# Kernel tuning notes

Measured on AMD Instinct MI355X. Metric: run time of the kernel, lower is better.

Reference implementation:

```python
import jax, jax.numpy as jnp
import numpy as np

N_NODES = 100000
N_EDGES = 1600000
N_GRAPHS = 512
IN_DIM, HID_DIM, OUT_DIM = 128, 256, 128
EPS = 0.0  # PyG GINConv default eps (train_eps=False)


def setup_inputs() -> dict:
    key = jax.random.key(0)
    ks = jax.random.split(key, 9)
    x = jax.random.normal(ks[0], (N_NODES, IN_DIM), dtype=jnp.float32)
    edge_index = jax.random.randint(ks[1], (2, N_EDGES), 0, N_NODES, dtype=jnp.int64)
    batch_ids = jnp.sort(jax.random.randint(ks[2], (N_NODES,), 0, N_GRAPHS, dtype=jnp.int64))
    s1 = 1.0 / np.sqrt(IN_DIM)
    s2 = 1.0 / np.sqrt(HID_DIM)
    W1 = jax.random.normal(ks[3], (IN_DIM, HID_DIM), dtype=jnp.float32) * s1
    b1 = jax.random.normal(ks[4], (HID_DIM,), dtype=jnp.float32) * s1
    W2 = jax.random.normal(ks[5], (HID_DIM, HID_DIM), dtype=jnp.float32) * s2
    b2 = jax.random.normal(ks[6], (HID_DIM,), dtype=jnp.float32) * s2
    Wo = jax.random.normal(ks[7], (HID_DIM, OUT_DIM), dtype=jnp.float32) * s2
    bo = jax.random.normal(ks[8], (OUT_DIM,), dtype=jnp.float32) * s2
    return {"x": x, "edge_index": edge_index, "batch_ids": batch_ids,
            "W1": W1, "b1": b1, "W2": W2, "b2": b2, "Wo": Wo, "bo": bo}


def reference(x, edge_index, batch_ids, W1, b1, W2, b2, Wo, bo):
    src, dst = edge_index[0], edge_index[1]
    # GIN aggregation: sum of neighbor features scattered to destination nodes
    agg = jax.ops.segment_sum(x[src], dst, num_segments=N_NODES)  # [N, in]
    h = (1.0 + EPS) * x + agg
    # GIN MLP: Linear -> ReLU -> Linear -> ReLU
    h = jax.nn.relu(h @ W1 + b1)
    h = jax.nn.relu(h @ W2 + b2)
    out = h @ Wo + bo  # output_layer
    # global_add_pool over graphs
    pooled = jax.ops.segment_sum(out, batch_ids, num_segments=N_GRAPHS)  # [G, out]
    return pooled
```

## Files before the change

### kernel.cpp

```cpp
#include <hip/hip_runtime.h>

#define N_NODES  100000
#define M_PAD    100096
#define N_EDGES  1600000
#define N_GRAPHS 512
#define IN_DIM   128
#define HID_DIM  256
#define OUT_DIM  128

#define NB       782
#define BCAP     3072
#define CHUNK    2048
#define BKB      ((N_EDGES + CHUNK - 1) / CHUNK)

typedef __bf16 bf16x8 __attribute__((ext_vector_type(8)));
typedef __bf16 bf16x4 __attribute__((ext_vector_type(4)));
typedef __bf16 bf16x2 __attribute__((ext_vector_type(2)));
typedef float  f32x4  __attribute__((ext_vector_type(4)));

#define WP_L2_BASE 32768
#define WP_L3_BASE 98304
#define WP_TOTAL   131072

#define R_X    (N_NODES * IN_DIM / 4)
#define R_APAD ((M_PAD - N_NODES) * IN_DIM / 4)
#define R_WP   WP_TOTAL
#define R_OUT  (N_GRAPHS * OUT_DIM / 4)
#define R_CUR  NB
#define R_TOTAL (R_X + R_APAD + R_WP + R_OUT + R_CUR)

__global__ __launch_bounds__(256) void init_kernel(const float* __restrict__ x,
                                                   const float* __restrict__ W1,
                                                   const float* __restrict__ W2,
                                                   const float* __restrict__ Wo,
                                                   __bf16* __restrict__ xb,
                                                   __bf16* __restrict__ Apad,
                                                   __bf16* __restrict__ Wp,
                                                   float* __restrict__ outbuf,
                                                   int* __restrict__ gcursor) {
    long long i = (long long)blockIdx.x * blockDim.x + threadIdx.x;
    if (i < R_X) {
        float4 v = ((const float4*)x)[i];
        bf16x4 h;
        h.x = (__bf16)v.x; h.y = (__bf16)v.y; h.z = (__bf16)v.z; h.w = (__bf16)v.w;
        ((bf16x4*)xb)[i] = h;
        return;
    }
    i -= R_X;
    if (i < R_APAD) {
        bf16x4 z; z.x = (__bf16)0.f; z.y = (__bf16)0.f; z.z = (__bf16)0.f; z.w = (__bf16)0.f;
        ((bf16x4*)Apad)[i] = z;
        return;
    }
    i -= R_APAD;
    if (i < R_WP) {
        int idx = (int)i;
        const float* src;
        int K, Nn, base;
        if (idx < WP_L2_BASE)      { src = W1; K = 128; Nn = 256; base = 0; }
        else if (idx < WP_L3_BASE) { src = W2; K = 256; Nn = 256; base = WP_L2_BASE; }
        else                       { src = Wo; K = 256; Nn = 128; base = WP_L3_BASE; }
        int r0 = idx - base;
        int slabElems = 32 * K;
        int j = r0 / slabElems;
        int r = r0 % slabElems;
        int KS = K / 32;
        int p = r >> 9;
        int lane = (r >> 3) & 63;
        int e = r & 7;
        int s = p % KS, t = p / KS;
        int quad = lane >> 4, l16 = lane & 15;
        int n = j * 32 + t * 16 + l16;
        int k = s * 32 + quad * 8 + e;
        Wp[idx] = (__bf16)src[(size_t)k * Nn + n];
        return;
    }
    i -= R_WP;
    if (i < R_OUT) {
        ((float4*)outbuf)[i] = make_float4(0.f, 0.f, 0.f, 0.f);
        return;
    }
    i -= R_OUT;
    if (i < R_CUR) gcursor[i] = 0;
}

__global__ __launch_bounds__(256) void bucket_v2_kernel(const int* __restrict__ ei,
                                                        int* __restrict__ gcursor,
                                                        unsigned* __restrict__ pairBuf) {
    __shared__ int lcnt[NB];
    __shared__ int lbase[NB];
    const int tid = threadIdx.x;
    const int e0 = blockIdx.x * CHUNK;

    for (int b = tid; b < NB; b += 256) lcnt[b] = 0;
    __syncthreads();

    for (int i = tid; i < CHUNK; i += 256) {
        int e = e0 + i;
        if (e < N_EDGES) atomicAdd(&lcnt[ei[N_EDGES + e] >> 7], 1);
    }
    __syncthreads();

    for (int b = tid; b < NB; b += 256) {
        int c = lcnt[b];
        lbase[b] = c ? atomicAdd(&gcursor[b], c) : 0;
        lcnt[b] = 0;
    }
    __syncthreads();

    for (int i = tid; i < CHUNK; i += 256) {
        int e = e0 + i;
        if (e < N_EDGES) {
            int s = ei[e];
            int d = ei[N_EDGES + e];
            int b = d >> 7;
            int pos = lbase[b] + atomicAdd(&lcnt[b], 1);
            if (pos < BCAP)
                pairBuf[(size_t)b * BCAP + pos] = (unsigned)s | ((unsigned)(d & 127) << 17);
        }
    }
}

__global__ __launch_bounds__(256) void passB_kernel(const unsigned* __restrict__ pairBuf,
                                                    const int* __restrict__ gcursor,
                                                    int* __restrict__ nbr,
                                                    int* __restrict__ offsets,
                                                    int* __restrict__ deg) {
    __shared__ int lcnt[128];
    __shared__ int loffs[128];
    __shared__ int lcur[128];
    const int b = blockIdx.x;
    const int tid = threadIdx.x;
    const int node0 = b << 7;
    const int cnt = min(gcursor[b], BCAP);
    const int base = b * BCAP;
    const unsigned* pb = pairBuf + (size_t)b * BCAP;

    if (tid < 128) { lcnt[tid] = 0; lcur[tid] = 0; }
    __syncthreads();

    for (int i = tid; i < cnt; i += 256)
        atomicAdd(&lcnt[pb[i] >> 17], 1);
    __syncthreads();

    if (tid < 128) loffs[tid] = lcnt[tid];
    __syncthreads();
    for (int st = 1; st < 128; st <<= 1) {
        int add = (tid < 128 && tid >= st) ? loffs[tid - st] : 0;
        __syncthreads();
        if (tid < 128) loffs[tid] += add;
        __syncthreads();
    }
    int excl = 0;
    if (tid < 128) {
        excl = loffs[tid] - lcnt[tid];
        int node = node0 + tid;
        if (node < N_NODES) {
            deg[node] = lcnt[tid];
            offsets[node] = base + excl;
        }
    }
    __syncthreads();
    if (tid < 128) loffs[tid] = excl;
    __syncthreads();

    for (int i = tid; i < cnt; i += 256) {
        unsigned u = pb[i];
        int dl = u >> 17;
        int slot = atomicAdd(&lcur[dl], 1);
        nbr[base + loffs[dl] + slot] = (int)(u & 0x1FFFF);
    }
}

__global__ __launch_bounds__(256) void aggregate_kernel(const __bf16* __restrict__ xb,
                                                        const int* __restrict__ offsets,
                                                        const int* __restrict__ deg,
                                                        const int* __restrict__ nbr,
                                                        __bf16* __restrict__ A) {
    int v = blockIdx.x * 4 + (threadIdx.x >> 6);
    v = __builtin_amdgcn_readfirstlane(v);
    int lane = threadIdx.x & 63;
    if (v >= N_NODES) return;
    int off = offsets[v];
    int len = deg[v];
    const int c0 = lane * 2;
    bf16x2 self = *(const bf16x2*)(xb + (size_t)v * IN_DIM + c0);
    float ax = (float)self.x, ay = (float)self.y;

    int addr = off + lane;
    if (addr > NB * BCAP - 1) addr = NB * BCAP - 1;
    int myidx = nbr[addr];

    int lim = len < 64 ? len : 64;
    int j = 0;
    for (; j + 8 <= lim; j += 8) {
        int s0 = __shfl(myidx, j + 0, 64);
        int s1 = __shfl(myidx, j + 1, 64);
        int s2 = __shfl(myidx, j + 2, 64);
        int s3 = __shfl(myidx, j + 3, 64);
        int s4 = __shfl(myidx, j + 4, 64);
        int s5 = __shfl(myidx, j + 5, 64);
        int s6 = __shfl(myidx, j + 6, 64);
        int s7 = __shfl(myidx, j + 7, 64);
        bf16x2 v0 = *(const bf16x2*)(xb + (size_t)s0 * IN_DIM + c0);
        bf16x2 v1 = *(const bf16x2*)(xb + (size_t)s1 * IN_DIM + c0);
        bf16x2 v2 = *(const bf16x2*)(xb + (size_t)s2 * IN_DIM + c0);
        bf16x2 v3 = *(const bf16x2*)(xb + (size_t)s3 * IN_DIM + c0);
        bf16x2 v4 = *(const bf16x2*)(xb + (size_t)s4 * IN_DIM + c0);
        bf16x2 v5 = *(const bf16x2*)(xb + (size_t)s5 * IN_DIM + c0);
        bf16x2 v6 = *(const bf16x2*)(xb + (size_t)s6 * IN_DIM + c0);
        bf16x2 v7 = *(const bf16x2*)(xb + (size_t)s7 * IN_DIM + c0);
        ax += (float)v0.x + (float)v1.x + (float)v2.x + (float)v3.x
            + (float)v4.x + (float)v5.x + (float)v6.x + (float)v7.x;
        ay += (float)v0.y + (float)v1.y + (float)v2.y + (float)v3.y
            + (float)v4.y + (float)v5.y + (float)v6.y + (float)v7.y;
    }
    for (; j < lim; ++j) {
        int s = __shfl(myidx, j, 64);
        bf16x2 vv = *(const bf16x2*)(xb + (size_t)s * IN_DIM + c0);
        ax += (float)vv.x;
        ay += (float)vv.y;
    }
    for (; j < len; ++j) {
        int s = nbr[off + j];
        bf16x2 vv = *(const bf16x2*)(xb + (size_t)s * IN_DIM + c0);
        ax += (float)vv.x;
        ay += (float)vv.y;
    }
    bf16x2 h;
    h.x = (__bf16)ax;
    h.y = (__bf16)ay;
    *(bf16x2*)(A + (size_t)v * IN_DIM + c0) = h;
}

__device__ __forceinline__ void load_group_p(const __bf16* __restrict__ p, int lane,
                                             bf16x8* __restrict__ dst) {
    #pragma unroll
    for (int e = 0; e < 8; ++e)
        dst[e] = *(const bf16x8*)(p + (e * 64 + lane) * 8);
}

__device__ __forceinline__ void store_H(__bf16* __restrict__ H, int j, int quad, int l16,
                                        const f32x4 (&acc)[2][2], float bt0, float bt1) {
    const int c7 = l16 & 7;
    const int ch = l16 >> 3;
    #pragma unroll
    for (int i = 0; i < 2; ++i)
        #pragma unroll
        for (int t = 0; t < 2; ++t) {
            const float bb = t ? bt1 : bt0;
            #pragma unroll
            for (int rr = 0; rr < 4; ++rr) {
                int row = i * 16 + quad * 4 + rr;
                int cidx = (j * 4 + t * 2 + ch + row) & 31;
                float v = fmaxf(acc[i][t][rr] + bb, 0.f);
                H[row * 256 + cidx * 8 + c7] = (__bf16)v;
            }
        }
}

__global__ __launch_bounds__(64) void mlp_fused(const __bf16* __restrict__ A,
                                                const __bf16* __restrict__ Wp,
                                                const float* __restrict__ b1,
                                                const float* __restrict__ b2,
                                                const float* __restrict__ bo,
                                                float* __restrict__ out,
                                                const int* __restrict__ batch) {
    __shared__ __bf16 H[32 * 256];

    const int lane = threadIdx.x;
    const int quad = lane >> 4, l16 = lane & 15;
    const size_t mblk = (size_t)blockIdx.x * 32;
    const int r0g = (int)mblk;
    int gfirst = (r0g < N_NODES) ? batch[r0g] : -2;
    int glast  = (r0g + 31 < N_NODES) ? batch[r0g + 31] : -1;

    bf16x8 a[2][8];
    bf16x8 buf0[8];
    bf16x8 buf1[8];

    const __bf16* wp = Wp;
    load_group_p(wp, lane, buf0);

    #pragma unroll
    for (int i = 0; i < 2; ++i)
        #pragma unroll
        for (int s = 0; s < 4; ++s)
            a[i][s] = *(const bf16x8*)(A + (mblk + i * 16 + l16) * IN_DIM + s * 32 + quad * 8);

    #pragma unroll 1
    for (int j = 0; j < 8; j += 2) {
        {
            load_group_p(wp + 4096, lane, buf1);
            float bt0 = b1[j * 32 + l16];
            float bt1 = b1[j * 32 + 16 + l16];
            f32x4 acc[2][2] = {};
            #pragma unroll
            for (int p = 0; p < 8; ++p) {
                const int t = p >> 2, s = p & 3;
                acc[0][t] = __builtin_amdgcn_mfma_f32_16x16x32_bf16(a[0][s], buf0[p], acc[0][t], 0, 0, 0);
                acc[1][t] = __builtin_amdgcn_mfma_f32_16x16x32_bf16(a[1][s], buf0[p], acc[1][t], 0, 0, 0);
            }
            store_H(H, j, quad, l16, acc, bt0, bt1);
        }
        {
            load_group_p(wp + 8192, lane, buf0);
            float bt0 = b1[(j + 1) * 32 + l16];
            float bt1 = b1[(j + 1) * 32 + 16 + l16];
            f32x4 acc[2][2] = {};
            #pragma unroll
            for (int p = 0; p < 8; ++p) {
                const int t = p >> 2, s = p & 3;
                acc[0][t] = __builtin_amdgcn_mfma_f32_16x16x32_bf16(a[0][s], buf1[p], acc[0][t], 0, 0, 0);
                acc[1][t] = __builtin_amdgcn_mfma_f32_16x16x32_bf16(a[1][s], buf1[p], acc[1][t], 0, 0, 0);
            }
            store_H(H, j + 1, quad, l16, acc, bt0, bt1);
        }
        wp += 8192;
    }
    __syncthreads();

    #pragma unroll
    for (int i = 0; i < 2; ++i)
        #pragma unroll
        for (int s = 0; s < 8; ++s) {
            int row = i * 16 + l16;
            a[i][s] = *(const bf16x8*)(H + row * 256 + (((s * 4 + quad) + row) & 31) * 8);
        }
    __syncthreads();

    #pragma unroll 1
    for (int j = 0; j < 8; ++j) {
        load_group_p(wp + 4096, lane, buf1);
        float bt0 = b2[j * 32 + l16];
        float bt1 = b2[j * 32 + 16 + l16];
        f32x4 acc[2][2] = {};
        #pragma unroll
        for (int p = 0; p < 8; ++p) {
            acc[0][0] = __builtin_amdgcn_mfma_f32_16x16x32_bf16(a[0][p], buf0[p], acc[0][0], 0, 0, 0);
            acc[1][0] = __builtin_amdgcn_mfma_f32_16x16x32_bf16(a[1][p], buf0[p], acc[1][0], 0, 0, 0);
        }
        load_group_p(wp + 8192, lane, buf0);
        #pragma unroll
        for (int p = 0; p < 8; ++p) {
            acc[0][1] = __builtin_amdgcn_mfma_f32_16x16x32_bf16(a[0][p], buf1[p], acc[0][1], 0, 0, 0);
            acc[1][1] = __builtin_amdgcn_mfma_f32_16x16x32_bf16(a[1][p], buf1[p], acc[1][1], 0, 0, 0);
        }
        store_H(H, j, quad, l16, acc, bt0, bt1);
        wp += 8192;
    }
    __syncthreads();

    #pragma unroll
    for (int i = 0; i < 2; ++i)
        #pragma unroll
        for (int s = 0; s < 8; ++s) {
            int row = i * 16 + l16;
            a[i][s] = *(const bf16x8*)(H + row * 256 + (((s * 4 + quad) + row) & 31) * 8);
        }

    #pragma unroll 1
    for (int j = 0; j < 4; ++j) {
        load_group_p(wp + 4096, lane, buf1);
        float bt0 = bo[j * 32 + l16];
        float bt1 = bo[j * 32 + 16 + l16];
        f32x4 acc[2][2] = {};
        #pragma unroll
        for (int p = 0; p < 8; ++p) {
            acc[0][0] = __builtin_amdgcn_mfma_f32_16x16x32_bf16(a[0][p], buf0[p], acc[0][0], 0, 0, 0);
            acc[1][0] = __builtin_amdgcn_mfma_f32_16x16x32_bf16(a[1][p], buf0[p], acc[1][0], 0, 0, 0);
        }
        load_group_p(wp + 8192, lane, buf0);
        #pragma unroll
        for (int p = 0; p < 8; ++p) {
            acc[0][1] = __builtin_amdgcn_mfma_f32_16x16x32_bf16(a[0][p], buf1[p], acc[0][1], 0, 0, 0);
            acc[1][1] = __builtin_amdgcn_mfma_f32_16x16x32_bf16(a[1][p], buf1[p], acc[1][1], 0, 0, 0);
        }

        if (gfirst == glast) {
            #pragma unroll
            for (int t = 0; t < 2; ++t) {
                float sum = 0.f;
                #pragma unroll
                for (int i = 0; i < 2; ++i)
                    #pragma unroll
                    for (int rr = 0; rr < 4; ++rr) sum += acc[i][t][rr];
                sum += __shfl_xor(sum, 16, 64);
                sum += __shfl_xor(sum, 32, 64);
                if (quad == 0) {
                    int c = j * 32 + t * 16 + l16;
                    float bb = t ? bt1 : bt0;
                    atomicAdd(out + (size_t)gfirst * OUT_DIM + c, sum + 32.f * bb);
                }
            }
        } else {
            #pragma unroll
            for (int i = 0; i < 2; ++i)
                #pragma unroll
                for (int rr = 0; rr < 4; ++rr) {
                    int m = r0g + i * 16 + quad * 4 + rr;
                    if (m < N_NODES) {
                        int g = batch[m];
                        #pragma unroll
                        for (int t = 0; t < 2; ++t) {
                            int c = j * 32 + t * 16 + l16;
                            float bb = t ? bt1 : bt0;
                            atomicAdd(out + (size_t)g * OUT_DIM + c, acc[i][t][rr] + bb);
                        }
                    }
                }
        }
        wp += 8192;
    }
}

extern "C" void kernel_launch(void* const* d_in, const int* in_sizes, int n_in,
                              void* d_out, int out_size, void* d_ws, size_t ws_size,
                              hipStream_t stream) {
    const float* x  = (const float*)d_in[0];
    const int*   ei = (const int*)d_in[1];
    const int*   bi = (const int*)d_in[2];
    const float* W1 = (const float*)d_in[3];
    const float* b1 = (const float*)d_in[4];
    const float* W2 = (const float*)d_in[5];
    const float* b2 = (const float*)d_in[6];
    const float* Wo = (const float*)d_in[7];
    const float* bo = (const float*)d_in[8];
    float* out = (float*)d_out;

    __bf16* A  = (__bf16*)d_ws;
    __bf16* xb = A + (size_t)M_PAD * IN_DIM;
    __bf16* Wp = xb + (size_t)N_NODES * IN_DIM;
    unsigned* pairBuf = (unsigned*)(Wp + WP_TOTAL);
    int* nbr      = (int*)(pairBuf + (size_t)NB * BCAP);
    int* offsets  = nbr + (size_t)NB * BCAP;
    int* deg      = offsets + N_NODES;
    int* gcursor  = deg + N_NODES;

    init_kernel<<<(R_TOTAL + 255) / 256, 256, 0, stream>>>(
        x, W1, W2, Wo, xb, A + (size_t)N_NODES * IN_DIM, Wp, out, gcursor);

    bucket_v2_kernel<<<BKB, 256, 0, stream>>>(ei, gcursor, pairBuf);
    passB_kernel<<<NB, 256, 0, stream>>>(pairBuf, gcursor, nbr, offsets, deg);

    aggregate_kernel<<<(N_NODES + 3) / 4, 256, 0, stream>>>(xb, offsets, deg, nbr, A);

    mlp_fused<<<M_PAD / 32, 64, 0, stream>>>(A, Wp, b1, b2, bo, out, bi);
}
```

Baseline: 290.0 us.

## Stage MLP weights through shared memory and widen row tiles per wave

The fused MLP kernel now uses two waves per block, each handling 64 rows instead of 32. Weight fragments are cooperatively loaded into a double-buffered LDS ring, with __syncthreads between stages, instead of every wave loading them straight from global memory. This is meant to halve weight traffic per row and to reuse each fragment across more MFMAs. In exchange it roughly doubles register use for A fragments and accumulators, and adds a block barrier on every weight stage.

New measurement: 336.5 us. +16.0%, slower.

```diff
diff --git a/kernel.cpp b/kernel.cpp
--- a/kernel.cpp
+++ b/kernel.cpp
@@ -233,19 +233,59 @@
     *(bf16x2*)(A + (size_t)v * IN_DIM + c0) = h;
 }
 
-__device__ __forceinline__ void load_group_p(const __bf16* __restrict__ p, int lane,
-                                             bf16x8* __restrict__ dst) {
+#define MLP_ROWS_W  64
+#define MLP_WAVES   2
+#define MLP_ROWS_B  (MLP_ROWS_W * MLP_WAVES)
+
+__device__ __forceinline__ void stage_issue(const __bf16* __restrict__ g, int wid, int lane,
+                                            bf16x8* __restrict__ r) {
+    const __bf16* p = g + wid * 2048 + lane * 8;
+    #pragma unroll
+    for (int c = 0; c < 4; ++c)
+        r[c] = *(const bf16x8*)(p + c * 512);
+}
+
+__device__ __forceinline__ void stage_write(__bf16* __restrict__ lb, int wid, int lane,
+                                            const bf16x8* __restrict__ r) {
+    __bf16* p = lb + wid * 2048 + lane * 8;
+    #pragma unroll
+    for (int c = 0; c < 4; ++c)
+        *(bf16x8*)(p + c * 512) = r[c];
+}
+
+__device__ __forceinline__ void read_frags(const __bf16* __restrict__ lb, int lane,
+                                           bf16x8* __restrict__ f) {
     #pragma unroll
     for (int e = 0; e < 8; ++e)
-        dst[e] = *(const bf16x8*)(p + (e * 64 + lane) * 8);
+        f[e] = *(const bf16x8*)(lb + (e * 64 + lane) * 8);
+}
+
+__device__ __forceinline__ void mfma_L1(const bf16x8 (&a)[4][8], const bf16x8* __restrict__ f,
+                                        f32x4 (&acc)[4][2]) {
+    #pragma unroll
+    for (int p = 0; p < 8; ++p) {
+        const int t = p >> 2, s = p & 3;
+        #pragma unroll
+        for (int i = 0; i < 4; ++i)
+            acc[i][t] = __builtin_amdgcn_mfma_f32_16x16x32_bf16(a[i][s], f[p], acc[i][t], 0, 0, 0);
+    }
+}
+
+__device__ __forceinline__ void mfma_K256(const bf16x8 (&a)[4][8], const bf16x8* __restrict__ f,
+                                          f32x4 (&acc)[4][2], int t) {
+    #pragma unroll
+    for (int p = 0; p < 8; ++p)
+        #pragma unroll
+        for (int i = 0; i < 4; ++i)
+            acc[i][t] = __builtin_amdgcn_mfma_f32_16x16x32_bf16(a[i][p], f[p], acc[i][t], 0, 0, 0);
 }
 
 __device__ __forceinline__ void store_H(__bf16* __restrict__ H, int j, int quad, int l16,
-                                        const f32x4 (&acc)[2][2], float bt0, float bt1) {
+                                        const f32x4 (&acc)[4][2], float bt0, float bt1) {
     const int c7 = l16 & 7;
     const int ch = l16 >> 3;
     #pragma unroll
-    for (int i = 0; i < 2; ++i)
+    for (int i = 0; i < 4; ++i)
         #pragma unroll
         for (int t = 0; t < 2; ++t) {
             const float bb = t ? bt1 : bt0;
@@ -259,130 +299,116 @@
         }
 }
 
-__global__ __launch_bounds__(64) void mlp_fused(const __bf16* __restrict__ A,
-                                                const __bf16* __restrict__ Wp,
-                                                const float* __restrict__ b1,
-                                                const float* __restrict__ b2,
-                                                const float* __restrict__ bo,
-                                                float* __restrict__ out,
-                                                const int* __restrict__ batch) {
-    __shared__ __bf16 H[32 * 256];
-
-    const int lane = threadIdx.x;
+__global__ __launch_bounds__(128, 1) void mlp_fused(const __bf16* __restrict__ A,
+                                                    const __bf16* __restrict__ Wp,
+                                                    const float* __restrict__ b1,
+                                                    const float* __restrict__ b2,
+                                                    const float* __restrict__ bo,
+                                                    float* __restrict__ out,
+                                                    const int* __restrict__ batch) {
+    __shared__ __align__(16) __bf16 H[MLP_ROWS_B * 256];
+    __shared__ __align__(16) __bf16 WB[2][4096];
+
+    const int tid  = threadIdx.x;
+    const int wid  = tid >> 6;
+    const int lane = tid & 63;
     const int quad = lane >> 4, l16 = lane & 15;
-    const size_t mblk = (size_t)blockIdx.x * 32;
+    __bf16* Hw = H + wid * MLP_ROWS_W * 256;
+
+    const size_t mblk = (size_t)blockIdx.x * MLP_ROWS_B + wid * MLP_ROWS_W;
     const int r0g = (int)mblk;
     int gfirst = (r0g < N_NODES) ? batch[r0g] : -2;
-    int glast  = (r0g + 31 < N_NODES) ? batch[r0g + 31] : -1;
-
-    bf16x8 a[2][8];
-    bf16x8 buf0[8];
-    bf16x8 buf1[8];
-
-    const __bf16* wp = Wp;
-    load_group_p(wp, lane, buf0);
-
-    #pragma unroll
-    for (int i = 0; i < 2; ++i)
+    int glast  = (r0g + 63 < N_NODES) ? batch[r0g + 63] : -1;
+
+    bf16x8 a[4][8];
+    bf16x8 f[8];
+    bf16x8 st[4];
+
+    stage_issue(Wp, wid, lane, st);
+    #pragma unroll
+    for (int i = 0; i < 4; ++i)
         #pragma unroll
         for (int s = 0; s < 4; ++s)
             a[i][s] = *(const bf16x8*)(A + (mblk + i * 16 + l16) * IN_DIM + s * 32 + quad * 8);
+    stage_write(WB[0], wid, lane, st);
+    __syncthreads();
+
+    const __bf16* wp = Wp;
 
     #pragma unroll 1
-    for (int j = 0; j < 8; j += 2) {
-        {
-            load_group_p(wp + 4096, lane, buf1);
-            float bt0 = b1[j * 32 + l16];
-            float bt1 = b1[j * 32 + 16 + l16];
-            f32x4 acc[2][2] = {};
-            #pragma unroll
-            for (int p = 0; p < 8; ++p) {
-                const int t = p >> 2, s = p & 3;
-                acc[0][t] = __builtin_amdgcn_mfma_f32_16x16x32_bf16(a[0][s], buf0[p], acc[0][t], 0, 0, 0);
-                acc[1][t] = __builtin_amdgcn_mfma_f32_16x16x32_bf16(a[1][s], buf0[p], acc[1][t], 0, 0, 0);
-            }
-            store_H(H, j, quad, l16, acc, bt0, bt1);
-        }
-        {
-            load_group_p(wp + 8192, lane, buf0);
-            float bt0 = b1[(j + 1) * 32 + l16];
-            float bt1 = b1[(j + 1) * 32 + 16 + l16];
-            f32x4 acc[2][2] = {};
-            #pragma unroll
-            for (int p = 0; p < 8; ++p) {
-                const int t = p >> 2, s = p & 3;
-                acc[0][t] = __builtin_amdgcn_mfma_f32_16x16x32_bf16(a[0][s], buf1[p], acc[0][t], 0, 0, 0);
-                acc[1][t] = __builtin_amdgcn_mfma_f32_16x16x32_bf16(a[1][s], buf1[p], acc[1][t], 0, 0, 0);
-            }
-            store_H(H, j + 1, quad, l16, acc, bt0, bt1);
-        }
-        wp += 8192;
-    }
-    __syncthreads();
-
-    #pragma unroll
-    for (int i = 0; i < 2; ++i)
+    for (int j = 0; j < 8; ++j) {
+        stage_issue(wp + 4096, wid, lane, st);
+        read_frags(WB[j & 1], lane, f);
+        float bt0 = b1[j * 32 + l16];
+        float bt1 = b1[j * 32 + 16 + l16];
+        f32x4 acc[4][2] = {};
+        mfma_L1(a, f, acc);
+        store_H(Hw, j, quad, l16, acc, bt0, bt1);
+        stage_write(WB[(j + 1) & 1], wid, lane, st);
+        __syncthreads();
+        wp += 4096;
+    }
+
+    #pragma unroll
+    for (int i = 0; i < 4; ++i)
         #pragma unroll
         for (int s = 0; s < 8; ++s) {
             int row = i * 16 + l16;
-            a[i][s] = *(const bf16x8*)(H + row * 256 + (((s * 4 + quad) + row) & 31) * 8);
-        }
-    __syncthreads();
+            a[i][s] = *(const bf16x8*)(Hw + row * 256 + (((s * 4 + quad) + row) & 31) * 8);
+        }
 
     #pragma unroll 1
     for (int j = 0; j < 8; ++j) {
-        load_group_p(wp + 4096, lane, buf1);
+        f32x4 acc[4][2] = {};
+        stage_issue(wp + 4096, wid, lane, st);
+        read_frags(WB[0], lane, f);
+        mfma_K256(a, f, acc, 0);
+        stage_write(WB[1], wid, lane, st);
+        __syncthreads();
+        wp += 4096;
+        stage_issue(wp + 4096, wid, lane, st);
+        read_frags(WB[1], lane, f);
+        mfma_K256(a, f, acc, 1);
+        stage_write(WB[0], wid, lane, st);
+        __syncthreads();
+        wp += 4096;
         float bt0 = b2[j * 32 + l16];
         float bt1 = b2[j * 32 + 16 + l16];
-        f32x4 acc[2][2] = {};
-        #pragma unroll
-        for (int p = 0; p < 8; ++p) {
-            acc[0][0] = __builtin_amdgcn_mfma_f32_16x16x32_bf16(a[0][p], buf0[p], acc[0][0], 0, 0, 0);
-            acc[1][0] = __builtin_amdgcn_mfma_f32_16x16x32_bf16(a[1][p], buf0[p], acc[1][0], 0, 0, 0);
-        }
-        load_group_p(wp + 8192, lane, buf0);
-        #pragma unroll
-        for (int p = 0; p < 8; ++p) {
-            acc[0][1] = __builtin_amdgcn_mfma_f32_16x16x32_bf16(a[0][p], buf1[p], acc[0][1], 0, 0, 0);
-            acc[1][1] = __builtin_amdgcn_mfma_f32_16x16x32_bf16(a[1][p], buf1[p], acc[1][1], 0, 0, 0);
-        }
-        store_H(H, j, quad, l16, acc, bt0, bt1);
-        wp += 8192;
-    }
-    __syncthreads();
-
-    #pragma unroll
-    for (int i = 0; i < 2; ++i)
+        store_H(Hw, j, quad, l16, acc, bt0, bt1);
+    }
+
+    #pragma unroll
+    for (int i = 0; i < 4; ++i)
         #pragma unroll
         for (int s = 0; s < 8; ++s) {
             int row = i * 16 + l16;
-            a[i][s] = *(const bf16x8*)(H + row * 256 + (((s * 4 + quad) + row) & 31) * 8);
+            a[i][s] = *(const bf16x8*)(Hw + row * 256 + (((s * 4 + quad) + row) & 31) * 8);
         }
 
     #pragma unroll 1
     for (int j = 0; j < 4; ++j) {
-        load_group_p(wp + 4096, lane, buf1);
+        f32x4 acc[4][2] = {};
+        stage_issue(wp + 4096, wid, lane, st);
+        read_frags(WB[0], lane, f);
+        mfma_K256(a, f, acc, 0);
+        stage_write(WB[1], wid, lane, st);
+        __syncthreads();
+        wp += 4096;
+        stage_issue(wp + 4096, wid, lane, st);
+        read_frags(WB[1], lane, f);
+        mfma_K256(a, f, acc, 1);
+        stage_write(WB[0], wid, lane, st);
+        __syncthreads();
+        wp += 4096;
         float bt0 = bo[j * 32 + l16];
         float bt1 = bo[j * 32 + 16 + l16];
-        f32x4 acc[2][2] = {};
-        #pragma unroll
-        for (int p = 0; p < 8; ++p) {
-            acc[0][0] = __builtin_amdgcn_mfma_f32_16x16x32_bf16(a[0][p], buf0[p], acc[0][0], 0, 0, 0);
-            acc[1][0] = __builtin_amdgcn_mfma_f32_16x16x32_bf16(a[1][p], buf0[p], acc[1][0], 0, 0, 0);
-        }
-        load_group_p(wp + 8192, lane, buf0);
-        #pragma unroll
-        for (int p = 0; p < 8; ++p) {
-            acc[0][1] = __builtin_amdgcn_mfma_f32_16x16x32_bf16(a[0][p], buf1[p], acc[0][1], 0, 0, 0);
-            acc[1][1] = __builtin_amdgcn_mfma_f32_16x16x32_bf16(a[1][p], buf1[p], acc[1][1], 0, 0, 0);
-        }
 
         if (gfirst == glast) {
             #pragma unroll
             for (int t = 0; t < 2; ++t) {
                 float sum = 0.f;
                 #pragma unroll
-                for (int i = 0; i < 2; ++i)
+                for (int i = 0; i < 4; ++i)
                     #pragma unroll
                     for (int rr = 0; rr < 4; ++rr) sum += acc[i][t][rr];
                 sum += __shfl_xor(sum, 16, 64);
@@ -390,12 +416,12 @@
                 if (quad == 0) {
                     int c = j * 32 + t * 16 + l16;
                     float bb = t ? bt1 : bt0;
-                    atomicAdd(out + (size_t)gfirst * OUT_DIM + c, sum + 32.f * bb);
+                    atomicAdd(out + (size_t)gfirst * OUT_DIM + c, sum + 64.f * bb);
                 }
             }
         } else {
             #pragma unroll
-            for (int i = 0; i < 2; ++i)
+            for (int i = 0; i < 4; ++i)
                 #pragma unroll
                 for (int rr = 0; rr < 4; ++rr) {
                     int m = r0g + i * 16 + quad * 4 + rr;
@@ -410,7 +436,6 @@
                     }
                 }
         }
-        wp += 8192;
     }
 }
 
@@ -445,5 +470,5 @@
 
     aggregate_kernel<<<(N_NODES + 3) / 4, 256, 0, stream>>>(xb, offsets, deg, nbr, A);
 
-    mlp_fused<<<M_PAD / 32, 64, 0, stream>>>(A, Wp, b1, b2, bo, out, bi);
-}
+    mlp_fused<<<M_PAD / MLP_ROWS_B, MLP_WAVES * 64, 0, stream>>>(A, Wp, b1, b2, bo, out, bi);
+}
```

## Pack four waves per MLP block and deepen weight prefetch to two groups

Applied to the files above, without the earlier changes.

The fused MLP kernel now runs four independent waves per 256-thread block, each with its own 32-row slice and private LDS tile, instead of one 64-thread wave per block. Weight fragments are triple or quad buffered in registers so each step loads the groups two steps ahead, hiding global/L2 latency behind the MFMAs. The goal is fewer, larger blocks and more latency hiding. The cost is higher register pressure (launch bounds 256,2) and 64KB of LDS per block, which may limit occupancy. M_PAD is evenly divisible by 128, so the grid still covers every row.

New measurement: 298.3 us. 2.9% more time.

```diff
diff --git a/kernel.cpp b/kernel.cpp
--- a/kernel.cpp
+++ b/kernel.cpp
@@ -233,8 +233,12 @@
     *(bf16x2*)(A + (size_t)v * IN_DIM + c0) = h;
 }
 
-__device__ __forceinline__ void load_group_p(const __bf16* __restrict__ p, int lane,
-                                             bf16x8* __restrict__ dst) {
+#define MLP_WAVES   4
+#define MLP_ROWS_W  32
+#define MLP_ROWS_B  (MLP_WAVES * MLP_ROWS_W)
+
+__device__ __forceinline__ void load_group4(const __bf16* __restrict__ p, int lane,
+                                            bf16x8* __restrict__ dst) {
     #pragma unroll
     for (int e = 0; e < 8; ++e)
         dst[e] = *(const bf16x8*)(p + (e * 64 + lane) * 8);
@@ -259,65 +263,60 @@
         }
 }
 
-__global__ __launch_bounds__(64) void mlp_fused(const __bf16* __restrict__ A,
-                                                const __bf16* __restrict__ Wp,
-                                                const float* __restrict__ b1,
-                                                const float* __restrict__ b2,
-                                                const float* __restrict__ bo,
-                                                float* __restrict__ out,
-                                                const int* __restrict__ batch) {
-    __shared__ __bf16 H[32 * 256];
-
-    const int lane = threadIdx.x;
+__global__ __launch_bounds__(256, 2) void mlp_fused(const __bf16* __restrict__ A,
+                                                    const __bf16* __restrict__ Wp,
+                                                    const float* __restrict__ b1,
+                                                    const float* __restrict__ b2,
+                                                    const float* __restrict__ bo,
+                                                    float* __restrict__ out,
+                                                    const int* __restrict__ batch) {
+    __shared__ __align__(16) __bf16 H[MLP_WAVES][32 * 256];
+
+    const int tid  = threadIdx.x;
+    const int wid  = tid >> 6;
+    const int lane = tid & 63;
     const int quad = lane >> 4, l16 = lane & 15;
-    const size_t mblk = (size_t)blockIdx.x * 32;
+    __bf16* Hw = H[wid];
+
+    const size_t mblk = (size_t)blockIdx.x * MLP_ROWS_B + wid * MLP_ROWS_W;
     const int r0g = (int)mblk;
     int gfirst = (r0g < N_NODES) ? batch[r0g] : -2;
     int glast  = (r0g + 31 < N_NODES) ? batch[r0g + 31] : -1;
 
     bf16x8 a[2][8];
-    bf16x8 buf0[8];
-    bf16x8 buf1[8];
-
-    const __bf16* wp = Wp;
-    load_group_p(wp, lane, buf0);
-
+    bf16x8 w0[8], w1[8], w2[8], w3[8];
+
+    load_group4(Wp, lane, w0);
+    load_group4(Wp + 4096, lane, w1);
     #pragma unroll
     for (int i = 0; i < 2; ++i)
         #pragma unroll
         for (int s = 0; s < 4; ++s)
             a[i][s] = *(const bf16x8*)(A + (mblk + i * 16 + l16) * IN_DIM + s * 32 + quad * 8);
 
+#define L1_BODY(J, CW, PW)                                                              \
+    {                                                                                   \
+        load_group4(Wp + (size_t)((J) + 2) * 4096, lane, PW);                           \
+        float bt0 = b1[(J) * 32 + l16];                                                 \
+        float bt1 = b1[(J) * 32 + 16 + l16];                                            \
+        f32x4 acc[2][2] = {};                                                           \
+        _Pragma("unroll")                                                               \
+        for (int p = 0; p < 8; ++p) {                                                   \
+            const int t = p >> 2, s = p & 3;                                            \
+            acc[0][t] = __builtin_amdgcn_mfma_f32_16x16x32_bf16(a[0][s], CW[p], acc[0][t], 0, 0, 0); \
+            acc[1][t] = __builtin_amdgcn_mfma_f32_16x16x32_bf16(a[1][s], CW[p], acc[1][t], 0, 0, 0); \
+        }                                                                               \
+        store_H(Hw, (J), quad, l16, acc, bt0, bt1);                                     \
+    }
+
     #pragma unroll 1
-    for (int j = 0; j < 8; j += 2) {
-        {
-            load_group_p(wp + 4096, lane, buf1);
-            float bt0 = b1[j * 32 + l16];
-            float bt1 = b1[j * 32 + 16 + l16];
-            f32x4 acc[2][2] = {};
-            #pragma unroll
-            for (int p = 0; p < 8; ++p) {
-                const int t = p >> 2, s = p & 3;
-                acc[0][t] = __builtin_amdgcn_mfma_f32_16x16x32_bf16(a[0][s], buf0[p], acc[0][t], 0, 0, 0);
-                acc[1][t] = __builtin_amdgcn_mfma_f32_16x16x32_bf16(a[1][s], buf0[p], acc[1][t], 0, 0, 0);
-            }
-            store_H(H, j, quad, l16, acc, bt0, bt1);
-        }
-        {
-            load_group_p(wp + 8192, lane, buf0);
-            float bt0 = b1[(j + 1) * 32 + l16];
-            float bt1 = b1[(j + 1) * 32 + 16 + l16];
-            f32x4 acc[2][2] = {};
-            #pragma unroll
-            for (int p = 0; p < 8; ++p) {
-                const int t = p >> 2, s = p & 3;
-                acc[0][t] = __builtin_amdgcn_mfma_f32_16x16x32_bf16(a[0][s], buf1[p], acc[0][t], 0, 0, 0);
-                acc[1][t] = __builtin_amdgcn_mfma_f32_16x16x32_bf16(a[1][s], buf1[p], acc[1][t], 0, 0, 0);
-            }
-            store_H(H, j + 1, quad, l16, acc, bt0, bt1);
-        }
-        wp += 8192;
-    }
+    for (int j = 0; j < 8; j += 4) {
+        L1_BODY(j + 0, w0, w2)
+        L1_BODY(j + 1, w1, w3)
+        L1_BODY(j + 2, w2, w0)
+        L1_BODY(j + 3, w3, w1)
+    }
+#undef L1_BODY
     __syncthreads();
 
     #pragma unroll
@@ -325,29 +324,34 @@
         #pragma unroll
         for (int s = 0; s < 8; ++s) {
             int row = i * 16 + l16;
-            a[i][s] = *(const bf16x8*)(H + row * 256 + (((s * 4 + quad) + row) & 31) * 8);
+            a[i][s] = *(const bf16x8*)(Hw + row * 256 + (((s * 4 + quad) + row) & 31) * 8);
         }
-    __syncthreads();
+
+#define K256_BODY(GB, J, CE, CO, PE, PO, BIAS, TAIL)                                    \
+    {                                                                                   \
+        const __bf16* pf = Wp + (size_t)((GB) + 2 * (J) + 2) * 4096;                    \
+        load_group4(pf, lane, PE);                                                      \
+        load_group4(pf + 4096, lane, PO);                                               \
+        float bt0 = BIAS[(J) * 32 + l16];                                               \
+        float bt1 = BIAS[(J) * 32 + 16 + l16];                                          \
+        f32x4 acc[2][2] = {};                                                           \
+        _Pragma("unroll")                                                               \
+        for (int p = 0; p < 8; ++p) {                                                   \
+            acc[0][0] = __builtin_amdgcn_mfma_f32_16x16x32_bf16(a[0][p], CE[p], acc[0][0], 0, 0, 0); \
+            acc[1][0] = __builtin_amdgcn_mfma_f32_16x16x32_bf16(a[1][p], CE[p], acc[1][0], 0, 0, 0); \
+        }                                                                               \
+        _Pragma("unroll")                                                               \
+        for (int p = 0; p < 8; ++p) {                                                   \
+            acc[0][1] = __builtin_amdgcn_mfma_f32_16x16x32_bf16(a[0][p], CO[p], acc[0][1], 0, 0, 0); \
+            acc[1][1] = __builtin_amdgcn_mfma_f32_16x16x32_bf16(a[1][p], CO[p], acc[1][1], 0, 0, 0); \
+        }                                                                               \
+        TAIL                                                                            \
+    }
 
     #pragma unroll 1
-    for (int j = 0; j < 8; ++j) {
-        load_group_p(wp + 4096, lane, buf1);
-        float bt0 = b2[j * 32 + l16];
-        float bt1 = b2[j * 32 + 16 + l16];
-        f32x4 acc[2][2] = {};
-        #pragma unroll
-        for (int p = 0; p < 8; ++p) {
-            acc[0][0] = __builtin_amdgcn_mfma_f32_16x16x32_bf16(a[0][p], buf0[p], acc[0][0], 0, 0, 0);
-            acc[1][0] = __builtin_amdgcn_mfma_f32_16x16x32_bf16(a[1][p], buf0[p], acc[1][0], 0, 0, 0);
-        }
-        load_group_p(wp + 8192, lane, buf0);
-        #pragma unroll
-        for (int p = 0; p < 8; ++p) {
-            acc[0][1] = __builtin_amdgcn_mfma_f32_16x16x32_bf16(a[0][p], buf1[p], acc[0][1], 0, 0, 0);
-            acc[1][1] = __builtin_amdgcn_mfma_f32_16x16x32_bf16(a[1][p], buf1[p], acc[1][1], 0, 0, 0);
-        }
-        store_H(H, j, quad, l16, acc, bt0, bt1);
-        wp += 8192;
+    for (int j = 0; j < 8; j += 2) {
+        K256_BODY(8, j,     w0, w1, w2, w3, b2, store_H(Hw, j,     quad, l16, acc, bt0, bt1);)
+        K256_BODY(8, j + 1, w2, w3, w0, w1, b2, store_H(Hw, j + 1, quad, l16, acc, bt0, bt1);)
     }
     __syncthreads();
 
@@ -356,62 +360,51 @@
         #pragma unroll
         for (int s = 0; s < 8; ++s) {
             int row = i * 16 + l16;
-            a[i][s] = *(const bf16x8*)(H + row * 256 + (((s * 4 + quad) + row) & 31) * 8);
+            a[i][s] = *(const bf16x8*)(Hw + row * 256 + (((s * 4 + quad) + row) & 31) * 8);
         }
 
+#define L3_TAIL(J)                                                                      \
+    if (gfirst == glast) {                                                              \
+        _Pragma("unroll")                                                               \
+        for (int t = 0; t < 2; ++t) {                                                   \
+            float sum = 0.f;                                                            \
+            _Pragma("unroll")                                                           \
+            for (int i = 0; i < 2; ++i)                                                 \
+                _Pragma("unroll")                                                       \
+                for (int rr = 0; rr < 4; ++rr) sum += acc[i][t][rr];                    \
+            sum += __shfl_xor(sum, 16, 64);                                             \
+            sum += __shfl_xor(sum, 32, 64);                                             \
+            if (quad == 0) {                                                            \
+                int c = (J) * 32 + t * 16 + l16;                                        \
+                float bb = t ? bt1 : bt0;                                               \
+                atomicAdd(out + (size_t)gfirst * OUT_DIM + c, sum + 32.f * bb);         \
+            }                                                                           \
+        }                                                                               \
+    } else {                                                                            \
+        _Pragma("unroll")                                                               \
+        for (int i = 0; i < 2; ++i)                                                     \
+            _Pragma("unroll")                                                           \
+            for (int rr = 0; rr < 4; ++rr) {                                            \
+                int m = r0g + i * 16 + quad * 4 + rr;                                   \
+                if (m < N_NODES) {                                                      \
+                    int g = batch[m];                                                   \
+                    _Pragma("unroll")                                                   \
+                    for (int t = 0; t < 2; ++t) {                                       \
+                        int c = (J) * 32 + t * 16 + l16;                                \
+                        float bb = t ? bt1 : bt0;                                       \
+                        atomicAdd(out + (size_t)g * OUT_DIM + c, acc[i][t][rr] + bb);   \
+                    }                                                                   \
+                }                                                                       \
+            }                                                                           \
+    }
+
     #pragma unroll 1
-    for (int j = 0; j < 4; ++j) {
-        load_group_p(wp + 4096, lane, buf1);
-        float bt0 = bo[j * 32 + l16];
-        float bt1 = bo[j * 32 + 16 + l16];
-        f32x4 acc[2][2] = {};
-        #pragma unroll
-        for (int p = 0; p < 8; ++p) {
-            acc[0][0] = __builtin_amdgcn_mfma_f32_16x16x32_bf16(a[0][p], buf0[p], acc[0][0], 0, 0, 0);
-            acc[1][0] = __builtin_amdgcn_mfma_f32_16x16x32_bf16(a[1][p], buf0[p], acc[1][0], 0, 0, 0);
-        }
-        load_group_p(wp + 8192, lane, buf0);
-        #pragma unroll
-        for (int p = 0; p < 8; ++p) {
-            acc[0][1] = __builtin_amdgcn_mfma_f32_16x16x32_bf16(a[0][p], buf1[p], acc[0][1], 0, 0, 0);
-            acc[1][1] = __builtin_amdgcn_mfma_f32_16x16x32_bf16(a[1][p], buf1[p], acc[1][1], 0, 0, 0);
-        }
-
-        if (gfirst == glast) {
-            #pragma unroll
-            for (int t = 0; t < 2; ++t) {
-                float sum = 0.f;
-                #pragma unroll
-                for (int i = 0; i < 2; ++i)
-                    #pragma unroll
-                    for (int rr = 0; rr < 4; ++rr) sum += acc[i][t][rr];
-                sum += __shfl_xor(sum, 16, 64);
-                sum += __shfl_xor(sum, 32, 64);
-                if (quad == 0) {
-                    int c = j * 32 + t * 16 + l16;
-                    float bb = t ? bt1 : bt0;
-                    atomicAdd(out + (size_t)gfirst * OUT_DIM + c, sum + 32.f * bb);
-                }
-            }
-        } else {
-            #pragma unroll
-            for (int i = 0; i < 2; ++i)
-                #pragma unroll
-                for (int rr = 0; rr < 4; ++rr) {
-                    int m = r0g + i * 16 + quad * 4 + rr;
-                    if (m < N_NODES) {
-                        int g = batch[m];
-                        #pragma unroll
-                        for (int t = 0; t < 2; ++t) {
-                            int c = j * 32 + t * 16 + l16;
-                            float bb = t ? bt1 : bt0;
-                            atomicAdd(out + (size_t)g * OUT_DIM + c, acc[i][t][rr] + bb);
-                        }
-                    }
-                }
-        }
-        wp += 8192;
-    }
+    for (int j = 0; j < 4; j += 2) {
+        K256_BODY(24, j,     w0, w1, w2, w3, bo, L3_TAIL(j))
+        K256_BODY(24, j + 1, w2, w3, w0, w1, bo, L3_TAIL(j + 1))
+    }
+#undef K256_BODY
+#undef L3_TAIL
 }
 
 extern "C" void kernel_launch(void* const* d_in, const int* in_sizes, int n_in,
@@ -445,5 +438,5 @@
 
     aggregate_kernel<<<(N_NODES + 3) / 4, 256, 0, stream>>>(xb, offsets, deg, nbr, A);
 
-    mlp_fused<<<M_PAD / 32, 64, 0, stream>>>(A, Wp, b1, b2, bo, out, bi);
-}
+    mlp_fused<<<M_PAD / MLP_ROWS_B, MLP_WAVES * 64, 0, stream>>>(A, Wp, b1, b2, bo, out, bi);
+}
```

## Stage MLP weights through shared LDS via async global_load_lds with two waves per block

Applied to the files above, without the earlier changes.

The fused MLP kernel now runs two waves per block. The two waves cooperatively stream weight tiles into a double-buffered LDS region using global_load_lds DMA, so each wave no longer loads every weight fragment from global memory into its own registers. Biases are preloaded into LDS once. This halves the weight traffic per row and frees the registers that held the second buffer, which may allow more waves per CU. The cost is a barrier after every tile, which couples the two waves, and a larger LDS footprint per block.

Measured after the change: 308.9 us. 1.07x slower.

```diff
diff --git a/kernel.cpp b/kernel.cpp
--- a/kernel.cpp
+++ b/kernel.cpp
@@ -233,11 +233,27 @@
     *(bf16x2*)(A + (size_t)v * IN_DIM + c0) = h;
 }
 
-__device__ __forceinline__ void load_group_p(const __bf16* __restrict__ p, int lane,
-                                             bf16x8* __restrict__ dst) {
+#define MLP_WAVES   2
+#define MLP_ROWS_W  32
+#define MLP_ROWS_B  (MLP_WAVES * MLP_ROWS_W)
+
+#define GLOAD_LDS16(gp, lp)                                              \
+    __builtin_amdgcn_global_load_lds(                                    \
+        (const __attribute__((address_space(1))) void*)(gp),             \
+        (__attribute__((address_space(3))) void*)(lp), 16, 0, 0)
+
+__device__ __forceinline__ void stage_dma(const __bf16* __restrict__ g,
+                                          __bf16* __restrict__ l, int wid, int lane) {
+    #pragma unroll
+    for (int c = 0; c < 4; ++c)
+        GLOAD_LDS16(g + wid * 2048 + c * 512 + lane * 8, l + wid * 2048 + c * 512);
+}
+
+__device__ __forceinline__ void read_frags(const __bf16* __restrict__ lb, int lane,
+                                           bf16x8* __restrict__ f) {
     #pragma unroll
     for (int e = 0; e < 8; ++e)
-        dst[e] = *(const bf16x8*)(p + (e * 64 + lane) * 8);
+        f[e] = *(const bf16x8*)(lb + (e * 64 + lane) * 8);
 }
 
 __device__ __forceinline__ void store_H(__bf16* __restrict__ H, int j, int quad, int l16,
@@ -259,123 +275,127 @@
         }
 }
 
-__global__ __launch_bounds__(64) void mlp_fused(const __bf16* __restrict__ A,
-                                                const __bf16* __restrict__ Wp,
-                                                const float* __restrict__ b1,
-                                                const float* __restrict__ b2,
-                                                const float* __restrict__ bo,
-                                                float* __restrict__ out,
-                                                const int* __restrict__ batch) {
-    __shared__ __bf16 H[32 * 256];
-
-    const int lane = threadIdx.x;
+#define WAIT_BAR()  do {                                   \
+    asm volatile("s_waitcnt vmcnt(0)" ::: "memory");       \
+    __builtin_amdgcn_s_barrier();                          \
+} while (0)
+
+__global__ __launch_bounds__(128, 2) void mlp_fused(const __bf16* __restrict__ A,
+                                                    const __bf16* __restrict__ Wp,
+                                                    const float* __restrict__ b1,
+                                                    const float* __restrict__ b2,
+                                                    const float* __restrict__ bo,
+                                                    float* __restrict__ out,
+                                                    const int* __restrict__ batch) {
+    __shared__ __align__(16) __bf16 H[MLP_WAVES][32 * 256];
+    __shared__ __align__(16) __bf16 WB[2][4096];
+    __shared__ float LB[640];
+
+    const int tid  = threadIdx.x;
+    const int wid  = tid >> 6;
+    const int lane = tid & 63;
     const int quad = lane >> 4, l16 = lane & 15;
-    const size_t mblk = (size_t)blockIdx.x * 32;
+    __bf16* Hw = H[wid];
+
+    const size_t mblk = (size_t)blockIdx.x * MLP_ROWS_B + wid * MLP_ROWS_W;
     const int r0g = (int)mblk;
     int gfirst = (r0g < N_NODES) ? batch[r0g] : -2;
     int glast  = (r0g + 31 < N_NODES) ? batch[r0g + 31] : -1;
 
     bf16x8 a[2][8];
-    bf16x8 buf0[8];
-    bf16x8 buf1[8];
-
-    const __bf16* wp = Wp;
-    load_group_p(wp, lane, buf0);
-
+    bf16x8 f[8];
+
+    stage_dma(Wp, WB[0], wid, lane);
+    for (int t = tid; t < 640; t += 128) {
+        float v = (t < 256) ? b1[t] : (t < 512) ? b2[t - 256] : bo[t - 512];
+        LB[t] = v;
+    }
     #pragma unroll
     for (int i = 0; i < 2; ++i)
         #pragma unroll
         for (int s = 0; s < 4; ++s)
             a[i][s] = *(const bf16x8*)(A + (mblk + i * 16 + l16) * IN_DIM + s * 32 + quad * 8);
+    __syncthreads();
 
     #pragma unroll 1
-    for (int j = 0; j < 8; j += 2) {
-        {
-            load_group_p(wp + 4096, lane, buf1);
-            float bt0 = b1[j * 32 + l16];
-            float bt1 = b1[j * 32 + 16 + l16];
-            f32x4 acc[2][2] = {};
-            #pragma unroll
-            for (int p = 0; p < 8; ++p) {
-                const int t = p >> 2, s = p & 3;
-                acc[0][t] = __builtin_amdgcn_mfma_f32_16x16x32_bf16(a[0][s], buf0[p], acc[0][t], 0, 0, 0);
-                acc[1][t] = __builtin_amdgcn_mfma_f32_16x16x32_bf16(a[1][s], buf0[p], acc[1][t], 0, 0, 0);
-            }
-            store_H(H, j, quad, l16, acc, bt0, bt1);
-        }
-        {
-            load_group_p(wp + 8192, lane, buf0);
-            float bt0 = b1[(j + 1) * 32 + l16];
-            float bt1 = b1[(j + 1) * 32 + 16 + l16];
-            f32x4 acc[2][2] = {};
-            #pragma unroll
-            for (int p = 0; p < 8; ++p) {
-                const int t = p >> 2, s = p & 3;
-                acc[0][t] = __builtin_amdgcn_mfma_f32_16x16x32_bf16(a[0][s], buf1[p], acc[0][t], 0, 0, 0);
-                acc[1][t] = __builtin_amdgcn_mfma_f32_16x16x32_bf16(a[1][s], buf1[p], acc[1][t], 0, 0, 0);
-            }
-            store_H(H, j + 1, quad, l16, acc, bt0, bt1);
-        }
-        wp += 8192;
-    }
-    __syncthreads();
+    for (int j = 0; j < 8; ++j) {
+        stage_dma(Wp + (size_t)(j + 1) * 4096, WB[(j + 1) & 1], wid, lane);
+        read_frags(WB[j & 1], lane, f);
+        float bt0 = LB[j * 32 + l16];
+        float bt1 = LB[j * 32 + 16 + l16];
+        f32x4 acc[2][2] = {};
+        #pragma unroll
+        for (int p = 0; p < 8; ++p) {
+            const int t = p >> 2, s = p & 3;
+            acc[0][t] = __builtin_amdgcn_mfma_f32_16x16x32_bf16(a[0][s], f[p], acc[0][t], 0, 0, 0);
+            acc[1][t] = __builtin_amdgcn_mfma_f32_16x16x32_bf16(a[1][s], f[p], acc[1][t], 0, 0, 0);
+        }
+        store_H(Hw, j, quad, l16, acc, bt0, bt1);
+        WAIT_BAR();
+    }
 
     #pragma unroll
     for (int i = 0; i < 2; ++i)
         #pragma unroll
         for (int s = 0; s < 8; ++s) {
             int row = i * 16 + l16;
-            a[i][s] = *(const bf16x8*)(H + row * 256 + (((s * 4 + quad) + row) & 31) * 8);
-        }
-    __syncthreads();
+            a[i][s] = *(const bf16x8*)(Hw + row * 256 + (((s * 4 + quad) + row) & 31) * 8);
+        }
 
     #pragma unroll 1
     for (int j = 0; j < 8; ++j) {
-        load_group_p(wp + 4096, lane, buf1);
-        float bt0 = b2[j * 32 + l16];
-        float bt1 = b2[j * 32 + 16 + l16];
+        const __bf16* gbase = Wp + (size_t)(8 + 2 * j) * 4096;
         f32x4 acc[2][2] = {};
+        stage_dma(gbase + 4096, WB[1], wid, lane);
+        read_frags(WB[0], lane, f);
         #pragma unroll
         for (int p = 0; p < 8; ++p) {
-            acc[0][0] = __builtin_amdgcn_mfma_f32_16x16x32_bf16(a[0][p], buf0[p], acc[0][0], 0, 0, 0);
-            acc[1][0] = __builtin_amdgcn_mfma_f32_16x16x32_bf16(a[1][p], buf0[p], acc[1][0], 0, 0, 0);
-        }
-        load_group_p(wp + 8192, lane, buf0);
+            acc[0][0] = __builtin_amdgcn_mfma_f32_16x16x32_bf16(a[0][p], f[p], acc[0][0], 0, 0, 0);
+            acc[1][0] = __builtin_amdgcn_mfma_f32_16x16x32_bf16(a[1][p], f[p], acc[1][0], 0, 0, 0);
+        }
+        WAIT_BAR();
+        stage_dma(gbase + 8192, WB[0], wid, lane);
+        read_frags(WB[1], lane, f);
         #pragma unroll
         for (int p = 0; p < 8; ++p) {
-            acc[0][1] = __builtin_amdgcn_mfma_f32_16x16x32_bf16(a[0][p], buf1[p], acc[0][1], 0, 0, 0);
-            acc[1][1] = __builtin_amdgcn_mfma_f32_16x16x32_bf16(a[1][p], buf1[p], acc[1][1], 0, 0, 0);
-        }
-        store_H(H, j, quad, l16, acc, bt0, bt1);
-        wp += 8192;
-    }
-    __syncthreads();
+            acc[0][1] = __builtin_amdgcn_mfma_f32_16x16x32_bf16(a[0][p], f[p], acc[0][1], 0, 0, 0);
+            acc[1][1] = __builtin_amdgcn_mfma_f32_16x16x32_bf16(a[1][p], f[p], acc[1][1], 0, 0, 0);
+        }
+        float bt0 = LB[256 + j * 32 + l16];
+        float bt1 = LB[256 + j * 32 + 16 + l16];
+        store_H(Hw, j, quad, l16, acc, bt0, bt1);
+        WAIT_BAR();
+    }
 
     #pragma unroll
     for (int i = 0; i < 2; ++i)
         #pragma unroll
         for (int s = 0; s < 8; ++s) {
             int row = i * 16 + l16;
-            a[i][s] = *(const bf16x8*)(H + row * 256 + (((s * 4 + quad) + row) & 31) * 8);
+            a[i][s] = *(const bf16x8*)(Hw + row * 256 + (((s * 4 + quad) + row) & 31) * 8);
         }
 
     #pragma unroll 1
     for (int j = 0; j < 4; ++j) {
-        load_group_p(wp + 4096, lane, buf1);
-        float bt0 = bo[j * 32 + l16];
-        float bt1 = bo[j * 32 + 16 + l16];
+        const __bf16* gbase = Wp + (size_t)(24 + 2 * j) * 4096;
         f32x4 acc[2][2] = {};
+        stage_dma(gbase + 4096, WB[1], wid, lane);
+        read_frags(WB[0], lane, f);
         #pragma unroll
         for (int p = 0; p < 8; ++p) {
-            acc[0][0] = __builtin_amdgcn_mfma_f32_16x16x32_bf16(a[0][p], buf0[p], acc[0][0], 0, 0, 0);
-            acc[1][0] = __builtin_amdgcn_mfma_f32_16x16x32_bf16(a[1][p], buf0[p], acc[1][0], 0, 0, 0);
-        }
-        load_group_p(wp + 8192, lane, buf0);
+            acc[0][0] = __builtin_amdgcn_mfma_f32_16x16x32_bf16(a[0][p], f[p], acc[0][0], 0, 0, 0);
+            acc[1][0] = __builtin_amdgcn_mfma_f32_16x16x32_bf16(a[1][p], f[p], acc[1][0], 0, 0, 0);
+        }
+        WAIT_BAR();
+        stage_dma(gbase + 8192, WB[0], wid, lane);
+        read_frags(WB[1], lane, f);
         #pragma unroll
         for (int p = 0; p < 8; ++p) {
-            acc[0][1] = __builtin_amdgcn_mfma_f32_16x16x32_bf16(a[0][p], buf1[p], acc[0][1], 0, 0, 0);
-            acc[1][1] = __builtin_amdgcn_mfma_f32_16x16x32_bf16(a[1][p], buf1[p], acc[1][1], 0, 0, 0);
-        }
+            acc[0][1] = __builtin_amdgcn_mfma_f32_16x16x32_bf16(a[0][p], f[p], acc[0][1], 0, 0, 0);
+            acc[1][1] = __builtin_amdgcn_mfma_f32_16x16x32_bf16(a[1][p], f[p], acc[1][1], 0, 0, 0);
+        }
+        float bt0 = LB[512 + j * 32 + l16];
+        float bt1 = LB[512 + j * 32 + 16 + l16];
 
         if (gfirst == glast) {
             #pragma unroll
@@ -410,7 +430,7 @@
                     }
                 }
         }
-        wp += 8192;
+        WAIT_BAR();
     }
 }
 
@@ -445,5 +465,5 @@
 
     aggregate_kernel<<<(N_NODES + 3) / 4, 256, 0, stream>>>(xb, offsets, deg, nbr, A);
 
-    mlp_fused<<<M_PAD / 32, 64, 0, stream>>>(A, Wp, b1, b2, bo, out, bi);
-}
+    mlp_fused<<<M_PAD / MLP_ROWS_B, MLP_WAVES * 64, 0, stream>>>(A, Wp, b1, b2, bo, out, bi);
+}
```
